# Optimization experiments

Hardware: AMD Instinct MI355X
Metric: run time of the kernel (lower is better)

## Reference

```python
import jax, jax.numpy as jnp
import numpy as np

N_NODES = 100000


def _gcn_norm(edge_index, num_nodes):
    # add self loops, then symmetric normalization D^-1/2 (A+I) D^-1/2
    loops = jnp.arange(num_nodes, dtype=edge_index.dtype)
    src = jnp.concatenate([edge_index[0], loops])
    dst = jnp.concatenate([edge_index[1], loops])
    ones = jnp.ones(src.shape[0], dtype=jnp.float32)
    deg = jax.ops.segment_sum(ones, dst, num_segments=num_nodes)
    dinv = jnp.where(deg > 0, jax.lax.rsqrt(deg), 0.0)
    norm = dinv[src] * dinv[dst]  # [E+N]
    return src, dst, norm


def setup_inputs() -> dict:
    key = jax.random.key(0)
    k1, k2, k3, k4 = jax.random.split(key, 4)
    x = jax.random.normal(k1, (N_NODES, 512), dtype=jnp.float32)
    edge_index = jax.random.randint(k2, (2, 3200000), 0, N_NODES, dtype=jnp.int64)
    # SGConv linear: Linear(num_features=512, num_classes=40)
    W = jax.random.normal(k3, (40, 512), dtype=jnp.float32) / np.sqrt(512.0)
    b = jax.random.normal(k4, (40,), dtype=jnp.float32) * 0.01
    return {"x": x, "edge_index": edge_index, "W": W, "b": b}


def reference(x, edge_index, W, b):
    K = 2  # args.num_layers
    src, dst, norm = _gcn_norm(edge_index, N_NODES)
    h = x
    for _ in range(K):
        # SpMM: out[dst] += norm * h[src]
        h = jax.ops.segment_sum(norm[:, None] * h[src], dst, num_segments=N_NODES)
    logits = h @ W.T + b  # [N, num_classes]
    return jax.nn.log_softmax(logits, axis=1)
```

## Files before the change

### kernel.cpp

```cpp
#include <hip/hip_runtime.h>
#include <hip/hip_bf16.h>
#include <math.h>


#define NFEAT 512
#define NCLS  40
#define NBUCK_MAX 256
#define CAP   18432

typedef __attribute__((ext_vector_type(8))) short bf16x8;
typedef __attribute__((ext_vector_type(4))) float f32x4;

__device__ inline short f2bf(float f) {
    union { float f; unsigned u; } v; v.f = f;
    unsigned r = (v.u + 0x7FFFu + ((v.u >> 16) & 1u)) >> 16;
    return (short)r;
}
__device__ inline unsigned pack2bf(float a, float b) {
    return (unsigned)(unsigned short)f2bf(a) | ((unsigned)(unsigned short)f2bf(b) << 16);
}
__device__ inline float bflo(unsigned v) {
    union { unsigned u; float f; } r; r.u = v << 16; return r.f;
}
__device__ inline float bfhi(unsigned v) {
    union { unsigned u; float f; } r; r.u = v & 0xFFFF0000u; return r.f;
}


__global__ __launch_bounds__(256) void scat6_kernel(const int* __restrict__ src,
                                                    const int* __restrict__ dst,
                                                    int* __restrict__ bcursor,
                                                    unsigned* __restrict__ bco, int E) {
    __shared__ int h[NBUCK_MAX], h2[NBUCK_MAX], base[NBUCK_MAX];
    int t = threadIdx.x;
    h[t] = 0; h2[t] = 0;
    __syncthreads();
    int cb = blockIdx.x * 2048;
    int d[8], s[8];
    bool m[8];
    #pragma unroll
    for (int u = 0; u < 8; ++u) {
        int e = cb + u * 256 + t;
        m[u] = e < E;
        d[u] = m[u] ? __builtin_nontemporal_load(dst + e) : 0;
        s[u] = m[u] ? __builtin_nontemporal_load(src + e) : 0;
        if (m[u]) atomicAdd(&h[d[u] >> 9], 1);
    }
    __syncthreads();
    if (h[t]) base[t] = t * CAP + atomicAdd(&bcursor[t], h[t]);
    __syncthreads();
    #pragma unroll
    for (int u = 0; u < 8; ++u) {
        if (m[u]) {
            int b = d[u] >> 9;
            int lp = atomicAdd(&h2[b], 1);
            bco[base[b] + lp] = ((unsigned)s[u] << 9) | (unsigned)(d[u] & 511);
        }
    }
}


__global__ __launch_bounds__(256) void sortb2_kernel(const unsigned* __restrict__ bco,
                                                     const int* __restrict__ bcursor,
                                                     int4* __restrict__ rowinfo,
                                                     float* __restrict__ dinv,
                                                     int* __restrict__ csr_src, int N) {
    __shared__ int deg[512], ex[512], sc[256];
    int b = blockIdx.x, t = threadIdx.x;
    int lo = b * 512;
    int nn = N - lo; if (nn > 512) nn = 512;
    int ebeg = b * CAP;
    int ecnt = bcursor[b];

    deg[t] = 0; deg[t + 256] = 0;
    __syncthreads();
    for (int i = t; i < ecnt; i += 256)
        atomicAdd(&deg[bco[ebeg + i] & 511u], 1);
    __syncthreads();
    int a0 = deg[2 * t], a1 = deg[2 * t + 1];
    int ps = a0 + a1;
    sc[t] = ps;
    __syncthreads();
    for (int off = 1; off < 256; off <<= 1) {
        int u = (t >= off) ? sc[t - off] : 0;
        __syncthreads();
        sc[t] += u;
        __syncthreads();
    }
    int pb = sc[t] - ps;
    ex[2 * t] = pb; ex[2 * t + 1] = pb + a0;
    __syncthreads();
    for (int j = t; j < nn; j += 256) {
        float di = rsqrtf((float)(deg[j] + 1));
        int4 ri;
        ri.x = ebeg + ex[j];
        ri.y = deg[j];
        ri.z = __float_as_int(di);
        ri.w = 0;
        rowinfo[lo + j] = ri;
        dinv[lo + j]    = di;
    }
    __syncthreads();
    for (int i = t; i < ecnt; i += 256) {
        unsigned v = bco[ebeg + i];
        int p = atomicAdd(&ex[v & 511u], 1);
        csr_src[ebeg + p] = (int)(v >> 9);
    }
}


__global__ void wfrag_kernel(const float* __restrict__ W, short* __restrict__ wfrag) {
    int i = blockIdx.x * blockDim.x + threadIdx.x;
    if (i >= 16 * 3 * 64) return;
    int kc = i / 192, rem = i % 192, tile = rem / 64, lane = rem % 64;
    int c = tile * 16 + (lane & 15);
    int kbase = kc * 32 + ((lane >> 4) << 3);
    bf16x8 out;
    #pragma unroll
    for (int j = 0; j < 8; ++j) {
        float v = (c < NCLS) ? W[(size_t)c * NFEAT + kbase + j] : 0.f;
        out[j] = f2bf(v);
    }
    *(bf16x8*)(wfrag + (size_t)i * 8) = out;
}


__global__ __launch_bounds__(512) void gemm4_kernel(const float* __restrict__ x,
                                                    const short* __restrict__ wfrag,
                                                    unsigned short* __restrict__ zb, int n) {
    __shared__ short xl[2][128 * 40];
    int t = threadIdx.x;
    int w = t >> 6, l = t & 63;
    int lrow = l & 15, lk = l >> 4;
    int rowBase = blockIdx.x * 128;
    int srow = t >> 2, skq = t & 3;
    f32x4 acc0 = {0.f, 0.f, 0.f, 0.f}, acc1 = acc0, acc2 = acc0;
    const float* xrow = x + (size_t)(rowBase + srow) * NFEAT + skq * 8;
    bool srOK = (rowBase + srow) < n;
    int aoff = (w * 16 + lrow) * 40 + lk * 8;
    int doff = srow * 40 + skq * 8;

    {
        float4 v0 = make_float4(0.f, 0.f, 0.f, 0.f), v1 = v0;
        if (srOK) { const float4* xp = (const float4*)xrow; v0 = xp[0]; v1 = xp[1]; }
        bf16x8 bv;
        bv[0] = f2bf(v0.x); bv[1] = f2bf(v0.y); bv[2] = f2bf(v0.z); bv[3] = f2bf(v0.w);
        bv[4] = f2bf(v1.x); bv[5] = f2bf(v1.y); bv[6] = f2bf(v1.z); bv[7] = f2bf(v1.w);
        *(bf16x8*)&xl[0][doff] = bv;
    }
    __syncthreads();

    for (int kc = 0; kc < 16; ++kc) {
        int cur = kc & 1;
        float4 v0 = make_float4(0.f, 0.f, 0.f, 0.f), v1 = v0;
        if (kc < 15 && srOK) {
            const float4* xp = (const float4*)(xrow + (kc + 1) * 32);
            v0 = xp[0]; v1 = xp[1];
        }
        bf16x8 af = *(const bf16x8*)&xl[cur][aoff];
        const bf16x8* wf = (const bf16x8*)(wfrag + (size_t)kc * 3 * 64 * 8);
        bf16x8 b0 = wf[l];
        bf16x8 b1 = wf[64 + l];
        bf16x8 b2 = wf[128 + l];
        acc0 = __builtin_amdgcn_mfma_f32_16x16x32_bf16(af, b0, acc0, 0, 0, 0);
        acc1 = __builtin_amdgcn_mfma_f32_16x16x32_bf16(af, b1, acc1, 0, 0, 0);
        acc2 = __builtin_amdgcn_mfma_f32_16x16x32_bf16(af, b2, acc2, 0, 0, 0);
        if (kc < 15) {
            bf16x8 bv;
            bv[0] = f2bf(v0.x); bv[1] = f2bf(v0.y); bv[2] = f2bf(v0.z); bv[3] = f2bf(v0.w);
            bv[4] = f2bf(v1.x); bv[5] = f2bf(v1.y); bv[6] = f2bf(v1.z); bv[7] = f2bf(v1.w);
            *(bf16x8*)&xl[cur ^ 1][doff] = bv;
            __syncthreads();
        }
    }
    int r0 = rowBase + w * 16 + lk * 4;
    #pragma unroll
    for (int reg = 0; reg < 4; ++reg) {
        int row = r0 + reg;
        if (row < n) {
            unsigned short* zp = zb + (size_t)row * NCLS;
            zp[lrow]      = (unsigned short)f2bf(acc0[reg]);
            zp[16 + lrow] = (unsigned short)f2bf(acc1[reg]);
            if (lrow < 8) zp[32 + lrow] = (unsigned short)f2bf(acc2[reg]);
        }
    }
}


template <bool FINAL>
__global__ void spmm4_kernel(const unsigned short* __restrict__ in,
                             const int4* __restrict__ rowinfo,
                             const int* __restrict__ csr_src, const float* __restrict__ dinv,
                             const float* __restrict__ bias, void* __restrict__ outv, int n) {
    int wave = (int)((blockIdx.x * (size_t)blockDim.x + threadIdx.x) >> 6);
    int lane = threadIdx.x & 63;
    if (wave >= n) return;
    int d = wave;
    int half = lane >> 5, hl = lane & 31;
    bool lact = hl < (NCLS / 2);
    int4 ri = rowinfo[d];
    int beg = ri.x, tot = ri.y;
    float dd = __int_as_float(ri.z);

    float a0 = 0.f, a1 = 0.f;
    if (half == 0 && lact) {
        unsigned v = *(const unsigned*)(in + (size_t)d * NCLS + hl * 2);
        a0 = dd * bflo(v); a1 = dd * bfhi(v);
    }

    for (int base = 0; base < tot; base += 64) {
        int cnt = tot - base; if (cnt > 64) cnt = 64;
        int sl = 0; float wl = 0.f;
        if (lane < cnt) { sl = csr_src[beg + base + lane]; wl = dinv[sl]; }
        int np = (cnt + 1) >> 1;
        int j = 0;
        for (; j + 4 <= np; j += 4) {
            int e0 = 2 * j + half, e1 = e0 + 2, e2 = e0 + 4, e3 = e0 + 6;
            int   s0 = __shfl(sl, e0, 64), s1 = __shfl(sl, e1, 64);
            int   s2 = __shfl(sl, e2, 64), s3 = __shfl(sl, e3, 64);
            float w0 = __shfl(wl, e0, 64), w1 = __shfl(wl, e1, 64);
            float w2 = __shfl(wl, e2, 64), w3 = __shfl(wl, e3, 64);
            bool m0 = lact && (e0 < cnt), m1 = lact && (e1 < cnt);
            bool m2 = lact && (e2 < cnt), m3 = lact && (e3 < cnt);
            unsigned v0 = 0, v1 = 0, v2 = 0, v3 = 0;
            if (m0) v0 = *(const unsigned*)(in + (size_t)s0 * NCLS + hl * 2);
            if (m1) v1 = *(const unsigned*)(in + (size_t)s1 * NCLS + hl * 2);
            if (m2) v2 = *(const unsigned*)(in + (size_t)s2 * NCLS + hl * 2);
            if (m3) v3 = *(const unsigned*)(in + (size_t)s3 * NCLS + hl * 2);
            if (m0) { a0 += w0 * bflo(v0); a1 += w0 * bfhi(v0); }
            if (m1) { a0 += w1 * bflo(v1); a1 += w1 * bfhi(v1); }
            if (m2) { a0 += w2 * bflo(v2); a1 += w2 * bfhi(v2); }
            if (m3) { a0 += w3 * bflo(v3); a1 += w3 * bfhi(v3); }
        }
        for (; j < np; ++j) {
            int e = 2 * j + half;
            int   s = __shfl(sl, e, 64);
            float w = __shfl(wl, e, 64);
            if (lact && e < cnt) {
                unsigned v = *(const unsigned*)(in + (size_t)s * NCLS + hl * 2);
                a0 += w * bflo(v); a1 += w * bfhi(v);
            }
        }
    }
    a0 += __shfl_xor(a0, 32, 64);
    a1 += __shfl_xor(a1, 32, 64);
    a0 *= dd; a1 *= dd;

    if (!FINAL) {
        if (half == 0 && lact) {
            unsigned short* ob = (unsigned short*)outv;
            *(unsigned*)(ob + (size_t)d * NCLS + hl * 2) = pack2bf(a0, a1);
        }
    } else {
        float2 bb = lact ? ((const float2*)bias)[hl] : make_float2(0.f, 0.f);
        float v0 = lact ? a0 + bb.x : -INFINITY;
        float v1 = lact ? a1 + bb.y : -INFINITY;
        float m = fmaxf(v0, v1);
        #pragma unroll
        for (int off = 16; off; off >>= 1) m = fmaxf(m, __shfl_xor(m, off, 64));
        float e0 = lact ? expf(v0 - m) : 0.f;
        float e1 = lact ? expf(v1 - m) : 0.f;
        float s = e0 + e1;
        #pragma unroll
        for (int off = 16; off; off >>= 1) s += __shfl_xor(s, off, 64);
        float lse = logf(s);
        if (half == 0 && lact) {
            float* out = (float*)outv;
            *(float2*)(out + (size_t)d * NCLS + hl * 2) = make_float2(v0 - m - lse, v1 - m - lse);
        }
    }
}


extern "C" void kernel_launch(void* const* d_in, const int* in_sizes, int n_in,
                              void* d_out, int out_size, void* d_ws, size_t ws_size,
                              hipStream_t stream) {
    const float* x  = (const float*)d_in[0];
    const int*   ei = (const int*)d_in[1];
    const float* W  = (const float*)d_in[2];
    const float* b  = (const float*)d_in[3];

    const int N = in_sizes[0] / NFEAT;
    const int E = in_sizes[1] / 2;
    const int* src = ei;
    const int* dst = ei + E;
    const int nbuck = (N + 511) / 512;

    char* p = (char*)d_ws;
    auto alloc = [&](size_t bytes) -> void* {
        void* r = (void*)p;
        p += (bytes + 255) & ~(size_t)255;
        return r;
    };
    int*      bcursor = (int*)     alloc((size_t)NBUCK_MAX * 4);
    int4*     rowinfo = (int4*)    alloc((size_t)N * 16);
    float*    dinv    = (float*)   alloc((size_t)N * 4);
    unsigned* bco     = (unsigned*)alloc((size_t)nbuck * CAP * 4);
    int*      csr_src = (int*)     alloc((size_t)nbuck * CAP * 4);
    short*    wfrag   = (short*)   alloc((size_t)16 * 3 * 64 * 8 * 2);
    unsigned short* zb = (unsigned short*)alloc((size_t)N * NCLS * 2);
    unsigned short* h1 = (unsigned short*)alloc((size_t)N * NCLS * 2);

    hipMemsetAsync(bcursor, 0, (size_t)NBUCK_MAX * 4, stream);

    int cb = (E + 2047) / 2048;
    scat6_kernel<<<cb, 256, 0, stream>>>(src, dst, bcursor, bco, E);
    sortb2_kernel<<<nbuck, 256, 0, stream>>>(bco, bcursor, rowinfo, dinv, csr_src, N);

    wfrag_kernel<<<12, 256, 0, stream>>>(W, wfrag);
    gemm4_kernel<<<(N + 127) / 128, 512, 0, stream>>>(x, wfrag, zb, N);

    int wb = (int)(((size_t)N * 64 + 255) / 256);
    spmm4_kernel<false><<<wb, 256, 0, stream>>>(zb, rowinfo, csr_src, dinv, b, h1, N);
    spmm4_kernel<true ><<<wb, 256, 0, stream>>>(h1, rowinfo, csr_src, dinv, b, d_out, N);
}
```

Baseline: 286.7 us.

## Prescale features by dinv and simplify SpMM to one lane per class

The GEMM epilogue now multiplies each output row by dinv[row], and the first SpMM stores its result scaled by dd*dd. With the source-side normalisation folded into the stored features, the SpMM no longer gathers dinv for every edge. The SpMM is also restructured: each wave handles one destination row with one lane per class. Column indices come from wave-uniform loads, so the old shuffle-based two-edges-per-wave scheme goes away. Lanes 40–63 read past the end of each row, so an extra zeroed padding row is allocated and cleared in the weight-fragment kernel. The cost is that 24 of 64 lanes do wasted 2-byte gathers, and the wave walks edges one at a time instead of two in parallel.

Result: slower. 293.4 us (+2.3%).

```diff
diff --git a/kernel.cpp b/kernel.cpp
--- a/kernel.cpp
+++ b/kernel.cpp
@@ -16,14 +16,8 @@
     unsigned r = (v.u + 0x7FFFu + ((v.u >> 16) & 1u)) >> 16;
     return (short)r;
 }
-__device__ inline unsigned pack2bf(float a, float b) {
-    return (unsigned)(unsigned short)f2bf(a) | ((unsigned)(unsigned short)f2bf(b) << 16);
-}
-__device__ inline float bflo(unsigned v) {
-    union { unsigned u; float f; } r; r.u = v << 16; return r.f;
-}
-__device__ inline float bfhi(unsigned v) {
-    union { unsigned u; float f; } r; r.u = v & 0xFFFF0000u; return r.f;
+__device__ inline float bf2f(unsigned short u) {
+    union { unsigned u; float f; } r; r.u = (unsigned)u << 16; return r.f;
 }
 
 
@@ -109,8 +103,14 @@
 }
 
 
-__global__ void wfrag_kernel(const float* __restrict__ W, short* __restrict__ wfrag) {
+__global__ void wfrag_kernel(const float* __restrict__ W, short* __restrict__ wfrag,
+                             unsigned short* __restrict__ zb,
+                             unsigned short* __restrict__ h1, int N) {
     int i = blockIdx.x * blockDim.x + threadIdx.x;
+    if (blockIdx.x == 0 && threadIdx.x < NCLS) {
+        zb[(size_t)N * NCLS + threadIdx.x] = 0;
+        h1[(size_t)N * NCLS + threadIdx.x] = 0;
+    }
     if (i >= 16 * 3 * 64) return;
     int kc = i / 192, rem = i % 192, tile = rem / 64, lane = rem % 64;
     int c = tile * 16 + (lane & 15);
@@ -125,8 +125,9 @@
 }
 
 
-__global__ __launch_bounds__(512) void gemm4_kernel(const float* __restrict__ x,
+__global__ __launch_bounds__(512) void gemm5_kernel(const float* __restrict__ x,
                                                     const short* __restrict__ wfrag,
+                                                    const float* __restrict__ dinv,
                                                     unsigned short* __restrict__ zb, int n) {
     __shared__ short xl[2][128 * 40];
     int t = threadIdx.x;
@@ -178,95 +179,68 @@
     for (int reg = 0; reg < 4; ++reg) {
         int row = r0 + reg;
         if (row < n) {
+            float sc = dinv[row];
             unsigned short* zp = zb + (size_t)row * NCLS;
-            zp[lrow]      = (unsigned short)f2bf(acc0[reg]);
-            zp[16 + lrow] = (unsigned short)f2bf(acc1[reg]);
-            if (lrow < 8) zp[32 + lrow] = (unsigned short)f2bf(acc2[reg]);
+            zp[lrow]      = (unsigned short)f2bf(acc0[reg] * sc);
+            zp[16 + lrow] = (unsigned short)f2bf(acc1[reg] * sc);
+            if (lrow < 8) zp[32 + lrow] = (unsigned short)f2bf(acc2[reg] * sc);
         }
     }
 }
 
 
 template <bool FINAL>
-__global__ void spmm4_kernel(const unsigned short* __restrict__ in,
-                             const int4* __restrict__ rowinfo,
-                             const int* __restrict__ csr_src, const float* __restrict__ dinv,
-                             const float* __restrict__ bias, void* __restrict__ outv, int n) {
-    int wave = (int)((blockIdx.x * (size_t)blockDim.x + threadIdx.x) >> 6);
+__global__ __launch_bounds__(256) void spmm5_kernel(const unsigned short* __restrict__ in,
+                                                    const int4* __restrict__ rowinfo,
+                                                    const int* __restrict__ csr,
+                                                    const float* __restrict__ bias,
+                                                    void* __restrict__ outv, int n) {
+    int wv = (int)((blockIdx.x * (size_t)blockDim.x + threadIdx.x) >> 6);
+    wv = __builtin_amdgcn_readfirstlane(wv);
+    if (wv >= n) return;
     int lane = threadIdx.x & 63;
-    if (wave >= n) return;
-    int d = wave;
-    int half = lane >> 5, hl = lane & 31;
-    bool lact = hl < (NCLS / 2);
-    int4 ri = rowinfo[d];
+
+    int4 ri = rowinfo[wv];
     int beg = ri.x, tot = ri.y;
     float dd = __int_as_float(ri.z);
 
-    float a0 = 0.f, a1 = 0.f;
-    if (half == 0 && lact) {
-        unsigned v = *(const unsigned*)(in + (size_t)d * NCLS + hl * 2);
-        a0 = dd * bflo(v); a1 = dd * bfhi(v);
-    }
-
-    for (int base = 0; base < tot; base += 64) {
-        int cnt = tot - base; if (cnt > 64) cnt = 64;
-        int sl = 0; float wl = 0.f;
-        if (lane < cnt) { sl = csr_src[beg + base + lane]; wl = dinv[sl]; }
-        int np = (cnt + 1) >> 1;
-        int j = 0;
-        for (; j + 4 <= np; j += 4) {
-            int e0 = 2 * j + half, e1 = e0 + 2, e2 = e0 + 4, e3 = e0 + 6;
-            int   s0 = __shfl(sl, e0, 64), s1 = __shfl(sl, e1, 64);
-            int   s2 = __shfl(sl, e2, 64), s3 = __shfl(sl, e3, 64);
-            float w0 = __shfl(wl, e0, 64), w1 = __shfl(wl, e1, 64);
-            float w2 = __shfl(wl, e2, 64), w3 = __shfl(wl, e3, 64);
-            bool m0 = lact && (e0 < cnt), m1 = lact && (e1 < cnt);
-            bool m2 = lact && (e2 < cnt), m3 = lact && (e3 < cnt);
-            unsigned v0 = 0, v1 = 0, v2 = 0, v3 = 0;
-            if (m0) v0 = *(const unsigned*)(in + (size_t)s0 * NCLS + hl * 2);
-            if (m1) v1 = *(const unsigned*)(in + (size_t)s1 * NCLS + hl * 2);
-            if (m2) v2 = *(const unsigned*)(in + (size_t)s2 * NCLS + hl * 2);
-            if (m3) v3 = *(const unsigned*)(in + (size_t)s3 * NCLS + hl * 2);
-            if (m0) { a0 += w0 * bflo(v0); a1 += w0 * bfhi(v0); }
-            if (m1) { a0 += w1 * bflo(v1); a1 += w1 * bfhi(v1); }
-            if (m2) { a0 += w2 * bflo(v2); a1 += w2 * bfhi(v2); }
-            if (m3) { a0 += w3 * bflo(v3); a1 += w3 * bfhi(v3); }
-        }
-        for (; j < np; ++j) {
-            int e = 2 * j + half;
-            int   s = __shfl(sl, e, 64);
-            float w = __shfl(wl, e, 64);
-            if (lact && e < cnt) {
-                unsigned v = *(const unsigned*)(in + (size_t)s * NCLS + hl * 2);
-                a0 += w * bflo(v); a1 += w * bfhi(v);
-            }
-        }
-    }
-    a0 += __shfl_xor(a0, 32, 64);
-    a1 += __shfl_xor(a1, 32, 64);
-    a0 *= dd; a1 *= dd;
+    float a = bf2f(in[(size_t)wv * NCLS + lane]);
+
+    int j = 0;
+    for (; j + 4 <= tot; j += 4) {
+        int s0 = csr[beg + j];
+        int s1 = csr[beg + j + 1];
+        int s2 = csr[beg + j + 2];
+        int s3 = csr[beg + j + 3];
+        float v0 = bf2f(in[(size_t)s0 * NCLS + lane]);
+        float v1 = bf2f(in[(size_t)s1 * NCLS + lane]);
+        float v2 = bf2f(in[(size_t)s2 * NCLS + lane]);
+        float v3 = bf2f(in[(size_t)s3 * NCLS + lane]);
+        a += v0; a += v1; a += v2; a += v3;
+    }
+    for (; j < tot; ++j) {
+        int s = csr[beg + j];
+        a += bf2f(in[(size_t)s * NCLS + lane]);
+    }
 
     if (!FINAL) {
-        if (half == 0 && lact) {
+        if (lane < NCLS) {
             unsigned short* ob = (unsigned short*)outv;
-            *(unsigned*)(ob + (size_t)d * NCLS + hl * 2) = pack2bf(a0, a1);
+            ob[(size_t)wv * NCLS + lane] = (unsigned short)f2bf(a * dd * dd);
         }
     } else {
-        float2 bb = lact ? ((const float2*)bias)[hl] : make_float2(0.f, 0.f);
-        float v0 = lact ? a0 + bb.x : -INFINITY;
-        float v1 = lact ? a1 + bb.y : -INFINITY;
-        float m = fmaxf(v0, v1);
+        float v = (lane < NCLS) ? a * dd + bias[lane] : -INFINITY;
+        float m = v;
         #pragma unroll
-        for (int off = 16; off; off >>= 1) m = fmaxf(m, __shfl_xor(m, off, 64));
-        float e0 = lact ? expf(v0 - m) : 0.f;
-        float e1 = lact ? expf(v1 - m) : 0.f;
-        float s = e0 + e1;
+        for (int off = 32; off; off >>= 1) m = fmaxf(m, __shfl_xor(m, off, 64));
+        float e = (lane < NCLS) ? expf(v - m) : 0.f;
+        float s = e;
         #pragma unroll
-        for (int off = 16; off; off >>= 1) s += __shfl_xor(s, off, 64);
+        for (int off = 32; off; off >>= 1) s += __shfl_xor(s, off, 64);
         float lse = logf(s);
-        if (half == 0 && lact) {
+        if (lane < NCLS) {
             float* out = (float*)outv;
-            *(float2*)(out + (size_t)d * NCLS + hl * 2) = make_float2(v0 - m - lse, v1 - m - lse);
+            out[(size_t)wv * NCLS + lane] = v - m - lse;
         }
     }
 }
@@ -295,11 +269,11 @@
     int*      bcursor = (int*)     alloc((size_t)NBUCK_MAX * 4);
     int4*     rowinfo = (int4*)    alloc((size_t)N * 16);
     float*    dinv    = (float*)   alloc((size_t)N * 4);
-    unsigned* bco     = (unsigned*)alloc((size_t)nbuck * CAP * 4);
-    int*      csr_src = (int*)     alloc((size_t)nbuck * CAP * 4);
+    unsigned* bco     = (unsigned*)alloc((size_t)nbuck * CAP * 4 + 64);
+    int*      csr_src = (int*)     alloc((size_t)nbuck * CAP * 4 + 64);
     short*    wfrag   = (short*)   alloc((size_t)16 * 3 * 64 * 8 * 2);
-    unsigned short* zb = (unsigned short*)alloc((size_t)N * NCLS * 2);
-    unsigned short* h1 = (unsigned short*)alloc((size_t)N * NCLS * 2);
+    unsigned short* zb = (unsigned short*)alloc(((size_t)N + 1) * NCLS * 2 + 256);
+    unsigned short* h1 = (unsigned short*)alloc(((size_t)N + 1) * NCLS * 2 + 256);
 
     hipMemsetAsync(bcursor, 0, (size_t)NBUCK_MAX * 4, stream);
 
@@ -307,10 +281,10 @@
     scat6_kernel<<<cb, 256, 0, stream>>>(src, dst, bcursor, bco, E);
     sortb2_kernel<<<nbuck, 256, 0, stream>>>(bco, bcursor, rowinfo, dinv, csr_src, N);
 
-    wfrag_kernel<<<12, 256, 0, stream>>>(W, wfrag);
-    gemm4_kernel<<<(N + 127) / 128, 512, 0, stream>>>(x, wfrag, zb, N);
+    wfrag_kernel<<<12, 256, 0, stream>>>(W, wfrag, zb, h1, N);
+    gemm5_kernel<<<(N + 127) / 128, 512, 0, stream>>>(x, wfrag, dinv, zb, N);
 
     int wb = (int)(((size_t)N * 64 + 255) / 256);
-    spmm4_kernel<false><<<wb, 256, 0, stream>>>(zb, rowinfo, csr_src, dinv, b, h1, N);
-    spmm4_kernel<true ><<<wb, 256, 0, stream>>>(h1, rowinfo, csr_src, dinv, b, d_out, N);
-}
+    spmm5_kernel<false><<<wb, 256, 0, stream>>>(zb, rowinfo, csr_src, b, h1, N);
+    spmm5_kernel<true ><<<wb, 256, 0, stream>>>(h1, rowinfo, csr_src, b, d_out, N);
+}
```
